# Kernel optimization log

Hardware: AMD Instinct MI355X
Metric: run time of the kernel (lower is better)

The kernel has to match this reference:

```python
import jax, jax.numpy as jnp
import numpy as np

N, E, IN, OUT, R, B = 20000, 640000, 128, 128, 65, 65
BN_EPS = 1e-5


def setup_inputs() -> dict:
    key = jax.random.key(0)
    ks = jax.random.split(key, 8)
    node_feats = jax.random.normal(ks[0], (N, IN), dtype=jnp.float32)
    src = jax.random.randint(ks[1], (E,), 0, N, dtype=jnp.int32)
    dst = jax.random.randint(ks[2], (E,), 0, N, dtype=jnp.int32)
    etype = jax.random.randint(ks[3], (E,), 0, R, dtype=jnp.int32)
    norm = jax.random.uniform(ks[4], (E, 1), dtype=jnp.float32)
    basis = jax.random.normal(ks[5], (B, IN, OUT), dtype=jnp.float32) * 0.05
    comp = jax.random.normal(ks[6], (R, B), dtype=jnp.float32) * 0.1
    h_bias = jnp.zeros((OUT,), dtype=jnp.float32)
    W_res = jax.random.normal(ks[7], (IN, OUT), dtype=jnp.float32) * 0.05
    b_res = jnp.zeros((OUT,), dtype=jnp.float32)
    gamma = jnp.ones((OUT,), dtype=jnp.float32)
    beta = jnp.zeros((OUT,), dtype=jnp.float32)
    return dict(node_feats=node_feats, src=src, dst=dst, etype=etype, norm=norm,
                basis=basis, comp=comp, h_bias=h_bias, W_res=W_res, b_res=b_res,
                gamma=gamma, beta=beta)


def reference(node_feats, src, dst, etype, norm, basis, comp, h_bias, W_res, b_res, gamma, beta):
    n, in_f = node_feats.shape
    r = comp.shape[0]
    # Basis decomposition: W_r = sum_b comp[r,b] * basis[b]  -> (R, in, out)
    W = jnp.einsum('rb,bio->rio', comp, basis)
    # Per-edge message x[src] * norm (norm is scalar per edge so it commutes
    # with the relation matmul). Aggregate per (dst, relation) first, then do
    # one dense relation-batched GEMM (mathematically identical to DGL's
    # per-edge transform + scatter-add, since everything is linear).
    msg = node_feats[src] * norm                       # (E, in)
    seg = dst.astype(jnp.int32) * r + etype            # combined (dst, rel) key
    S = jax.ops.segment_sum(msg, seg, num_segments=n * r).reshape(n, r, in_f)
    h = jnp.einsum('nri,rio->no', S, W) + h_bias       # (N, out)
    h = jax.nn.relu(h)                                 # conv activation (dropout p=0)
    # Residual branch: relu(Linear(x))
    h = h + jax.nn.relu(node_feats @ W_res + b_res)
    # BatchNorm1d (training mode: batch stats, biased variance)
    mean = jnp.mean(h, axis=0)
    var = jnp.var(h, axis=0)
    h = (h - mean) * jax.lax.rsqrt(var + BN_EPS) * gamma + beta
    return h
```

## Files before the change

kernel.cpp:

```cpp
#include <hip/hip_runtime.h>
#include <hip/hip_bf16.h>


#define N_NODES 20000
#define E_EDGES 640000
#define R_REL   65
#define TM      64
#define NB_RESID 313
#define MAX_TILES 10240
#define SCAT_CH 2560

typedef __attribute__((ext_vector_type(8))) short bf16x8;
typedef __attribute__((ext_vector_type(4))) float f32x4;
typedef __attribute__((ext_vector_type(4))) unsigned int u32x4;
typedef __attribute__((ext_vector_type(2))) unsigned int u32x2;

__device__ __forceinline__ unsigned short f2bf(float x) {
    union { float f; unsigned int u; } c; c.f = x;
    unsigned int b = c.u + 0x7fffu + ((c.u >> 16) & 1u);
    return (unsigned short)(b >> 16);
}
__device__ __forceinline__ float bf2f_lo(unsigned int u) {
    union { unsigned int u; float f; } c; c.u = u << 16; return c.f;
}
__device__ __forceinline__ float bf2f_hi(unsigned int u) {
    union { unsigned int u; float f; } c; c.u = u & 0xffff0000u; return c.f;
}
__device__ __forceinline__ void async16(const void* g, void* l) {
    __builtin_amdgcn_global_load_lds(
        (const __attribute__((address_space(1))) unsigned int*)g,
        (__attribute__((address_space(3))) unsigned int*)l, 16, 0, 0);
}
__device__ __forceinline__ int unperm(int p) {
    return (p & 64) + ((p & 3) << 4) + ((p >> 2) & 15);
}

__global__ void k_prep1(const float* __restrict__ comp, const float* __restrict__ basis,
                        float* __restrict__ W32, const int* __restrict__ et,
                        const int* __restrict__ dstA, int* __restrict__ ghist,
                        int* __restrict__ gh2, const float* __restrict__ node_feats,
                        unsigned short* __restrict__ node_bf) {
    __shared__ float lc[16 * 65];
    __shared__ int lh[R_REL];
    int b = blockIdx.x, t = threadIdx.x;
    if (b < 320) {
        int r0 = (b >> 6) * 16;
        int col = (b & 63) * 256 + t;
        for (int j = t; j < 16 * 65; j += 256) {
            int rr = r0 + j / 65;
            lc[j] = (rr < R_REL) ? comp[rr * 65 + (j % 65)] : 0.f;
        }
        __syncthreads();
        float acc[16];
#pragma unroll
        for (int j = 0; j < 16; ++j) acc[j] = 0.f;
        for (int k = 0; k < 65; ++k) {
            float v = basis[k * 16384 + col];
#pragma unroll
            for (int j = 0; j < 16; ++j) acc[j] += lc[j * 65 + k] * v;
        }
#pragma unroll
        for (int j = 0; j < 16; ++j) {
            int rr = r0 + j;
            if (rr < R_REL) W32[rr * 16384 + col] = acc[j];
        }
    } else if (b < 832) {
        if (t < R_REL) lh[t] = 0;
        __syncthreads();
        for (int i = (b - 320) * 256 + t; i < E_EDGES; i += 512 * 256) {
            atomicAdd(&lh[et[i]], 1);
            atomicAdd(&gh2[dstA[i]], 1);
        }
        __syncthreads();
        if (t < R_REL) atomicAdd(&ghist[t], lh[t]);
    } else {
        int i = (b - 832) * 256 + t;
        if (i < N_NODES * 32) {
            float4 v = reinterpret_cast<const float4*>(node_feats)[i];
            __hip_bfloat162 b0 = __float22bfloat162_rn(make_float2(v.x, v.y));
            __hip_bfloat162 b1 = __float22bfloat162_rn(make_float2(v.z, v.w));
            u32x2 pk;
            pk.x = *reinterpret_cast<unsigned int*>(&b0);
            pk.y = *reinterpret_cast<unsigned int*>(&b1);
            reinterpret_cast<u32x2*>(node_bf)[i] = pk;
        }
    }
}

__global__ void k_prep3(const int* __restrict__ gh2, int* __restrict__ cnt2,
                        int* __restrict__ seg, const int* __restrict__ ghist,
                        int* __restrict__ cnt, int* __restrict__ ntiles_p,
                        int* __restrict__ tile_rel, int* __restrict__ tile_start,
                        int* __restrict__ tile_len, const float* __restrict__ W32,
                        unsigned short* __restrict__ Wt, const float* __restrict__ Wresf,
                        unsigned short* __restrict__ Wrest) {
    int b = blockIdx.x, t = threadIdx.x;
    if (b < 80) {
        __shared__ int red[256];
        __shared__ int pref;
        int acc = 0;
        for (int i = t; i < b * 256; i += 256) acc += gh2[i];
        red[t] = acc;
        __syncthreads();
        for (int off = 128; off > 0; off >>= 1) {
            if (t < off) red[t] += red[t + off];
            __syncthreads();
        }
        if (t == 0) pref = red[0];
        __syncthreads();
        int i = b * 256 + t;
        int v = (i < N_NODES) ? gh2[i] : 0;
        red[t] = v;
        __syncthreads();
        for (int off = 1; off < 256; off <<= 1) {
            int x = (t >= off) ? red[t - off] : 0;
            __syncthreads();
            red[t] += x;
            __syncthreads();
        }
        int excl = red[t] - v + pref;
        if (i < N_NODES) {
            cnt2[i] = excl;
            seg[i] = excl;
            if (i == N_NODES - 1) seg[N_NODES] = excl + v;
        }
    } else if (b == 80) {
        __shared__ int base[R_REL + 1], tbase[R_REL + 1];
        int lane = t & 63;
        if (t < 64) {
            int v = ghist[lane];
            int x = v;
#pragma unroll
            for (int off = 1; off < 64; off <<= 1) {
                int y = __shfl_up(x, off);
                if (lane >= off) x += y;
            }
            base[lane] = x - v;
            if (lane == 63) {
                base[64] = x;
                base[65] = x + ghist[64];
            }
        }
        __syncthreads();
        if (t == 0) {
            int tb = 0;
            for (int r = 0; r < R_REL; ++r) {
                tbase[r] = tb;
                tb += (base[r + 1] - base[r] + TM - 1) / TM;
            }
            *ntiles_p = tb;
        }
        __syncthreads();
        if (t < R_REL) {
            cnt[t] = base[t];
            int s = base[t], e = base[t + 1], j = tbase[t];
            while (s < e) {
                int len = min(TM, e - s);
                tile_rel[j] = t; tile_start[j] = s; tile_len[j] = len;
                ++j; s += len;
            }
        }
    } else {
        __shared__ float tile[64][65];
        int bb = b - 81;
        const float* s; unsigned short* d; int sub;
        if (bb < R_REL * 4) { s = W32 + (size_t)(bb >> 2) * 16384; d = Wt + (size_t)(bb >> 2) * 16384; sub = bb & 3; }
        else { s = Wresf; d = Wrest; sub = bb - R_REL * 4; }
        int ot = (sub >> 1) & 1, itl = sub & 1;
        int tx = t & 63, ty = t >> 6;
        for (int it = 0; it < 16; ++it) {
            int i = ty + it * 4;
            tile[i][tx] = s[(itl * 64 + i) * 128 + ot * 64 + tx];
        }
        __syncthreads();
        for (int it = 0; it < 16; ++it) {
            int o = ty + it * 4;
            d[(ot * 64 + o) * 128 + itl * 64 + tx] = f2bf(tile[tx][o]);
        }
    }
}

__global__ void k_scatter2(const int* __restrict__ et, const int* __restrict__ srcA,
                           const int* __restrict__ dstA, const float* __restrict__ norm,
                           int* __restrict__ cnt, int* __restrict__ cnt2,
                           int* __restrict__ srcp, float* __restrict__ normp,
                           int* __restrict__ inv2) {
    __shared__ int lh[R_REL], lbase[R_REL];
    int c0 = blockIdx.x * SCAT_CH;
    int cend = min(c0 + SCAT_CH, E_EDGES);
    if (threadIdx.x < R_REL) lh[threadIdx.x] = 0;
    __syncthreads();
    for (int i = c0 + threadIdx.x; i < cend; i += 256) atomicAdd(&lh[et[i]], 1);
    __syncthreads();
    if (threadIdx.x < R_REL && lh[threadIdx.x] > 0)
        lbase[threadIdx.x] = atomicAdd(&cnt[threadIdx.x], lh[threadIdx.x]);
    __syncthreads();
    if (threadIdx.x < R_REL) lh[threadIdx.x] = 0;
    __syncthreads();
    for (int i = c0 + threadIdx.x; i < cend; i += 256) {
        int r = et[i];
        int p = lbase[r] + atomicAdd(&lh[r], 1);
        srcp[p] = srcA[i];
        normp[p] = norm[i];
        inv2[p] = atomicAdd(&cnt2[dstA[i]], 1);
    }
}

__global__ __launch_bounds__(256, 3) void k_conv_gemm(
    const int* __restrict__ tile_rel, const int* __restrict__ tile_start,
    const int* __restrict__ tile_len, const int* __restrict__ ntiles_p,
    const int* __restrict__ srcp, const float* __restrict__ normp,
    const unsigned short* __restrict__ node_bf,
    const unsigned short* __restrict__ Wt, const unsigned short* __restrict__ Wrest,
    const float* __restrict__ b_res, const int* __restrict__ inv2,
    unsigned short* __restrict__ t_out, float* __restrict__ resid) {
    __shared__ unsigned short Alds[64 * 128];
    __shared__ unsigned short Blds[128 * 128];
    __shared__ float snorm[64];
    __shared__ int sp2[64];
    int t = threadIdx.x;
    int w = t >> 6, lane = t & 63;
    int wr = (w >> 1) * 32, wc = (w & 1) * 64;
    int lrow = lane & 15, quad = lane >> 4;

    if (blockIdx.x < NB_RESID) {
        int row0 = blockIdx.x * 64;
        int nrows = min(64, N_NODES - row0);
#pragma unroll
        for (int it = 0; it < 8; ++it) {
            int j = t + 256 * it;
            int o = j >> 4, c = j & 15, cs = c ^ (o & 15);
            async16(Wrest + o * 128 + cs * 8, &Blds[o * 128 + c * 8]);
        }
#pragma unroll
        for (int it = 0; it < 4; ++it) {
            int j = t + 256 * it;
            int p = j >> 4, c = j & 15, cs = c ^ (p & 15);
            if (p < nrows)
                async16(node_bf + (size_t)(row0 + p) * 128 + cs * 8,
                        &Alds[p * 128 + c * 8]);
        }
        __syncthreads();
        f32x4 acc[2][4];
#pragma unroll
        for (int i = 0; i < 2; ++i)
#pragma unroll
            for (int j = 0; j < 4; ++j) acc[i][j] = (f32x4){0.f, 0.f, 0.f, 0.f};
#pragma unroll
        for (int ks = 0; ks < 4; ++ks) {
            int cs = (ks * 4 + quad) ^ lrow;
            bf16x8 af[2], bfr[4];
#pragma unroll
            for (int i = 0; i < 2; ++i)
                af[i] = *reinterpret_cast<const bf16x8*>(&Alds[(wr + i * 16 + lrow) * 128 + cs * 8]);
#pragma unroll
            for (int j = 0; j < 4; ++j)
                bfr[j] = *reinterpret_cast<const bf16x8*>(&Blds[(wc + j * 16 + lrow) * 128 + cs * 8]);
#pragma unroll
            for (int i = 0; i < 2; ++i)
#pragma unroll
                for (int j = 0; j < 4; ++j)
                    acc[i][j] = __builtin_amdgcn_mfma_f32_16x16x32_bf16(af[i], bfr[j], acc[i][j], 0, 0, 0);
        }
        float br0 = b_res[wc + lrow];
        float br1 = b_res[wc + 16 + lrow];
        float br2 = b_res[wc + 32 + lrow];
        float br3 = b_res[wc + 48 + lrow];
#pragma unroll
        for (int i = 0; i < 2; ++i) {
#pragma unroll
            for (int reg = 0; reg < 4; ++reg) {
                int grow = row0 + wr + i * 16 + quad * 4 + reg;
                if (grow < N_NODES) {
                    float4 v;
                    v.x = fmaxf(acc[i][0][reg] + br0, 0.f);
                    v.y = fmaxf(acc[i][1][reg] + br1, 0.f);
                    v.z = fmaxf(acc[i][2][reg] + br2, 0.f);
                    v.w = fmaxf(acc[i][3][reg] + br3, 0.f);
                    *reinterpret_cast<float4*>(resid + (size_t)grow * 128 + wc + lrow * 4) = v;
                }
            }
        }
        return;
    }

    int tid = blockIdx.x - NB_RESID;
    if (tid >= *ntiles_p) return;
    int r = tile_rel[tid], start = tile_start[tid], len = tile_len[tid];
    const unsigned short* Wr = Wt + (size_t)r * 16384;
#pragma unroll
    for (int it = 0; it < 8; ++it) {
        int j = t + 256 * it;
        int o = j >> 4, c = j & 15, cs = c ^ (o & 15);
        async16(Wr + o * 128 + cs * 8, &Blds[o * 128 + c * 8]);
    }
#pragma unroll
    for (int it = 0; it < 4; ++it) {
        int j = t + 256 * it;
        int p = j >> 4, c = j & 15, cs = c ^ (p & 15);
        if (p < len)
            async16(node_bf + (size_t)srcp[start + p] * 128 + cs * 8,
                    &Alds[p * 128 + c * 8]);
    }
    if (t < TM && t < len) {
        snorm[t] = normp[start + t];
        sp2[t] = inv2[start + t];
    }
    __syncthreads();

    f32x4 acc[2][4];
#pragma unroll
    for (int i = 0; i < 2; ++i)
#pragma unroll
        for (int j = 0; j < 4; ++j) acc[i][j] = (f32x4){0.f, 0.f, 0.f, 0.f};
#pragma unroll
    for (int ks = 0; ks < 4; ++ks) {
        int cs = (ks * 4 + quad) ^ lrow;
        bf16x8 af[2], bfr[4];
#pragma unroll
        for (int i = 0; i < 2; ++i)
            af[i] = *reinterpret_cast<const bf16x8*>(&Alds[(wr + i * 16 + lrow) * 128 + cs * 8]);
#pragma unroll
        for (int j = 0; j < 4; ++j)
            bfr[j] = *reinterpret_cast<const bf16x8*>(&Blds[(wc + j * 16 + lrow) * 128 + cs * 8]);
#pragma unroll
        for (int i = 0; i < 2; ++i)
#pragma unroll
            for (int j = 0; j < 4; ++j)
                acc[i][j] = __builtin_amdgcn_mfma_f32_16x16x32_bf16(af[i], bfr[j], acc[i][j], 0, 0, 0);
    }

#pragma unroll
    for (int i = 0; i < 2; ++i) {
        int m0 = wr + i * 16 + quad * 4;
#pragma unroll
        for (int reg = 0; reg < 4; ++reg) {
            int m = m0 + reg;
            if (m < len) {
                float nm = snorm[m];
                int p2 = sp2[m];
                float2 lo2 = make_float2(acc[i][0][reg] * nm, acc[i][1][reg] * nm);
                float2 hi2 = make_float2(acc[i][2][reg] * nm, acc[i][3][reg] * nm);
                __hip_bfloat162 blo = __float22bfloat162_rn(lo2);
                __hip_bfloat162 bhi = __float22bfloat162_rn(hi2);
                u32x2 st;
                st.x = *reinterpret_cast<unsigned int*>(&blo);
                st.y = *reinterpret_cast<unsigned int*>(&bhi);
                *reinterpret_cast<u32x2*>(t_out + (size_t)p2 * 128 + wc + lrow * 4) = st;
            }
        }
    }
}

__global__ __launch_bounds__(256) void k_reduce_fused(
    const unsigned short* __restrict__ t, const int* __restrict__ seg,
    const float* __restrict__ resid, const float* __restrict__ h_bias,
    float* __restrict__ h, float* __restrict__ colsum, float* __restrict__ colsumsq) {
    __shared__ float cs1[128], cs2[128], sbias[128];
    if (threadIdx.x < 128) {
        cs1[threadIdx.x] = 0.f; cs2[threadIdx.x] = 0.f;
        sbias[threadIdx.x] = h_bias[unperm(threadIdx.x)];
    }
    __syncthreads();
    int w = threadIdx.x >> 6, lane = threadIdx.x & 63;
    int g = lane >> 4, c = lane & 15;
    for (int k = 0; k < 4; ++k) {
        int d = blockIdx.x * 16 + k * 4 + w;
        int a = seg[d], b = seg[d + 1];
        float s[8];
#pragma unroll
        for (int kk = 0; kk < 8; ++kk) s[kk] = 0.f;
        int q = a + g;
        for (; q + 28 < b; q += 32) {
            u32x4 v0 = *reinterpret_cast<const u32x4*>(t + (size_t)q * 128 + c * 8);
            u32x4 v1 = *reinterpret_cast<const u32x4*>(t + (size_t)(q + 4) * 128 + c * 8);
            u32x4 v2 = *reinterpret_cast<const u32x4*>(t + (size_t)(q + 8) * 128 + c * 8);
            u32x4 v3 = *reinterpret_cast<const u32x4*>(t + (size_t)(q + 12) * 128 + c * 8);
            u32x4 v4 = *reinterpret_cast<const u32x4*>(t + (size_t)(q + 16) * 128 + c * 8);
            u32x4 v5 = *reinterpret_cast<const u32x4*>(t + (size_t)(q + 20) * 128 + c * 8);
            u32x4 v6 = *reinterpret_cast<const u32x4*>(t + (size_t)(q + 24) * 128 + c * 8);
            u32x4 v7 = *reinterpret_cast<const u32x4*>(t + (size_t)(q + 28) * 128 + c * 8);
#pragma unroll
            for (int kk = 0; kk < 4; ++kk) {
                s[2 * kk]     += bf2f_lo(v0[kk]) + bf2f_lo(v1[kk]) + bf2f_lo(v2[kk]) + bf2f_lo(v3[kk])
                               + bf2f_lo(v4[kk]) + bf2f_lo(v5[kk]) + bf2f_lo(v6[kk]) + bf2f_lo(v7[kk]);
                s[2 * kk + 1] += bf2f_hi(v0[kk]) + bf2f_hi(v1[kk]) + bf2f_hi(v2[kk]) + bf2f_hi(v3[kk])
                               + bf2f_hi(v4[kk]) + bf2f_hi(v5[kk]) + bf2f_hi(v6[kk]) + bf2f_hi(v7[kk]);
            }
        }
        for (; q < b; q += 4) {
            u32x4 v = *reinterpret_cast<const u32x4*>(t + (size_t)q * 128 + c * 8);
#pragma unroll
            for (int kk = 0; kk < 4; ++kk) {
                s[2 * kk]     += bf2f_lo(v[kk]);
                s[2 * kk + 1] += bf2f_hi(v[kk]);
            }
        }
#pragma unroll
        for (int kk = 0; kk < 8; ++kk) {
            s[kk] += __shfl_xor(s[kk], 16);
            s[kk] += __shfl_xor(s[kk], 32);
        }
        if (g == 0) {
            const float* rp = resid + (size_t)d * 128 + c * 8;
            float4 r0 = *reinterpret_cast<const float4*>(rp);
            float4 r1 = *reinterpret_cast<const float4*>(rp + 4);
            float rr[8] = {r0.x, r0.y, r0.z, r0.w, r1.x, r1.y, r1.z, r1.w};
            float v[8];
#pragma unroll
            for (int kk = 0; kk < 8; ++kk)
                v[kk] = fmaxf(s[kk] + sbias[c * 8 + kk], 0.f) + rr[kk];
            float* hp = h + (size_t)d * 128 + c * 8;
            *reinterpret_cast<float4*>(hp)     = make_float4(v[0], v[1], v[2], v[3]);
            *reinterpret_cast<float4*>(hp + 4) = make_float4(v[4], v[5], v[6], v[7]);
#pragma unroll
            for (int kk = 0; kk < 8; ++kk) {
                atomicAdd(&cs1[c * 8 + kk], v[kk]);
                atomicAdd(&cs2[c * 8 + kk], v[kk] * v[kk]);
            }
        }
    }
    __syncthreads();
    if (threadIdx.x < 128) {
        atomicAdd(&colsum[threadIdx.x], cs1[threadIdx.x]);
        atomicAdd(&colsumsq[threadIdx.x], cs2[threadIdx.x]);
    }
}

__global__ void k_bn(float* __restrict__ h, const float* __restrict__ colsum,
                     const float* __restrict__ colsumsq, const float* __restrict__ gamma,
                     const float* __restrict__ beta) {
    __shared__ float sc[128], sh[128], tile[8][128];
    int t = threadIdx.x;
    if (t < 128) {
        int n = unperm(t);
        float m = colsum[t] * (1.f / N_NODES);
        float var = colsumsq[t] * (1.f / N_NODES) - m * m;
        float s = gamma[n] * rsqrtf(var + 1e-5f);
        sc[t] = s;
        sh[t] = beta[n] - m * s;
    }
    __syncthreads();
    int r = t >> 5;
    int p0 = (t & 31) * 4;
    int n0 = (p0 & 64) + ((p0 >> 2) & 15);
    for (int row0 = blockIdx.x * 8; row0 < N_NODES; row0 += gridDim.x * 8) {
        int row = row0 + r;
        float4 v = make_float4(0.f, 0.f, 0.f, 0.f);
        if (row < N_NODES) v = *reinterpret_cast<float4*>(h + (size_t)row * 128 + p0);
        v.x = v.x * sc[p0] + sh[p0];
        v.y = v.y * sc[p0 + 1] + sh[p0 + 1];
        v.z = v.z * sc[p0 + 2] + sh[p0 + 2];
        v.w = v.w * sc[p0 + 3] + sh[p0 + 3];
        tile[r][n0]      = v.x;
        tile[r][n0 + 16] = v.y;
        tile[r][n0 + 32] = v.z;
        tile[r][n0 + 48] = v.w;
        __syncthreads();
        if (row < N_NODES)
            *reinterpret_cast<float4*>(h + (size_t)row * 128 + p0) =
                *reinterpret_cast<float4*>(&tile[r][p0]);
        __syncthreads();
    }
}

extern "C" void kernel_launch(void* const* d_in, const int* in_sizes, int n_in,
                              void* d_out, int out_size, void* d_ws, size_t ws_size,
                              hipStream_t stream) {
    (void)in_sizes; (void)n_in; (void)out_size; (void)ws_size;
    const float* node_feats = (const float*)d_in[0];
    const int* src    = (const int*)d_in[1];
    const int* dst    = (const int*)d_in[2];
    const int* etype  = (const int*)d_in[3];
    const float* norm = (const float*)d_in[4];
    const float* basis = (const float*)d_in[5];
    const float* comp  = (const float*)d_in[6];
    const float* h_bias = (const float*)d_in[7];
    const float* W_res  = (const float*)d_in[8];
    const float* b_res  = (const float*)d_in[9];
    const float* gamma  = (const float*)d_in[10];
    const float* beta   = (const float*)d_in[11];

    char* ws = (char*)d_ws;
    int* ghist      = (int*)(ws + 0);
    int* cnt        = (int*)(ws + 1024);
    int* ntiles_p   = (int*)(ws + 2048);
    float* colsum   = (float*)(ws + 2560);
    float* colsumsq = (float*)(ws + 3072);
    int* gh2        = (int*)(ws + 8192);
    int* tile_rel   = (int*)(ws + 88192);
    int* tile_start = (int*)(ws + 129152);
    int* tile_len   = (int*)(ws + 170112);
    unsigned short* Wt      = (unsigned short*)(ws + 211072);
    unsigned short* Wrest   = (unsigned short*)(ws + 2340992);
    unsigned short* node_bf = (unsigned short*)(ws + 2373760);
    int* srcp       = (int*)(ws + 7493760);
    float* normp    = (float*)(ws + 10053760);
    int* inv2       = (int*)(ws + 12613760);
    float* resid    = (float*)(ws + 15173760);
    int* seg        = (int*)(ws + 25413760);
    int* cnt2       = (int*)(ws + 25493776);
    const long T_BASE = 25573776L;
    float* W32      = (float*)(ws + T_BASE);
    unsigned short* t_buf = (unsigned short*)(ws + T_BASE);
    float* hacc = (float*)d_out;

    hipMemsetAsync(ws, 0, 88192, stream);
    k_prep1<<<3332, 256, 0, stream>>>(comp, basis, W32, etype, dst, ghist, gh2,
                                      node_feats, node_bf);
    k_prep3<<<345, 256, 0, stream>>>(gh2, cnt2, seg, ghist, cnt, ntiles_p,
                                     tile_rel, tile_start, tile_len,
                                     W32, Wt, W_res, Wrest);
    k_scatter2<<<(E_EDGES + SCAT_CH - 1) / SCAT_CH, 256, 0, stream>>>(
        etype, src, dst, norm, cnt, cnt2, srcp, normp, inv2);
    k_conv_gemm<<<NB_RESID + MAX_TILES, 256, 0, stream>>>(
        tile_rel, tile_start, tile_len, ntiles_p, srcp, normp, node_bf,
        Wt, Wrest, b_res, inv2, t_buf, resid);
    k_reduce_fused<<<N_NODES / 16, 256, 0, stream>>>(t_buf, seg, resid, h_bias,
                                                     hacc, colsum, colsumsq);
    k_bn<<<2500, 256, 0, stream>>>(hacc, colsum, colsumsq, gamma, beta);
}
```

Measured before the change: 323.0 us.

## Pack edge metadata and rebalance per-node reduction into edge-range sequential sweeps

The scatter now writes each edge's destination slot and norm as one packed 8-byte record, which the conv GEMM reads with a single load instead of two separate arrays. The per-node reduction is replaced by a kernel where each wavefront takes a fixed range of edge rows (found by binary search over seg) and walks it sequentially, emitting node rows as boundaries are crossed. Column statistics are kept in registers and added to shared memory only once per wavefront. Scatter chunk size is also reduced. This balances work across wavefronts regardless of node degree, at the cost of narrower 4-byte loads per lane and serial boundary handling.

```diff
diff --git a/kernel.cpp b/kernel.cpp
--- a/kernel.cpp
+++ b/kernel.cpp
@@ -8,7 +8,9 @@
 #define TM      64
 #define NB_RESID 313
 #define MAX_TILES 10240
-#define SCAT_CH 2560
+#define SCAT_CH 1024
+#define RED_BLOCKS 1000
+#define RL 160
 
 typedef __attribute__((ext_vector_type(8))) short bf16x8;
 typedef __attribute__((ext_vector_type(4))) float f32x4;
@@ -183,8 +185,7 @@
 __global__ void k_scatter2(const int* __restrict__ et, const int* __restrict__ srcA,
                            const int* __restrict__ dstA, const float* __restrict__ norm,
                            int* __restrict__ cnt, int* __restrict__ cnt2,
-                           int* __restrict__ srcp, float* __restrict__ normp,
-                           int* __restrict__ inv2) {
+                           int* __restrict__ srcp, unsigned int* __restrict__ em) {
     __shared__ int lh[R_REL], lbase[R_REL];
     int c0 = blockIdx.x * SCAT_CH;
     int cend = min(c0 + SCAT_CH, E_EDGES);
@@ -201,19 +202,21 @@
         int r = et[i];
         int p = lbase[r] + atomicAdd(&lh[r], 1);
         srcp[p] = srcA[i];
-        normp[p] = norm[i];
-        inv2[p] = atomicAdd(&cnt2[dstA[i]], 1);
+        int p2 = atomicAdd(&cnt2[dstA[i]], 1);
+        union { float f; unsigned int u; } c; c.f = norm[i];
+        u32x2 e; e.x = (unsigned int)p2; e.y = c.u;
+        *reinterpret_cast<u32x2*>(em + (size_t)p * 2) = e;
     }
 }
 
 __global__ __launch_bounds__(256, 3) void k_conv_gemm(
     const int* __restrict__ tile_rel, const int* __restrict__ tile_start,
     const int* __restrict__ tile_len, const int* __restrict__ ntiles_p,
-    const int* __restrict__ srcp, const float* __restrict__ normp,
+    const int* __restrict__ srcp, const unsigned int* __restrict__ em,
     const unsigned short* __restrict__ node_bf,
     const unsigned short* __restrict__ Wt, const unsigned short* __restrict__ Wrest,
-    const float* __restrict__ b_res, const int* __restrict__ inv2,
-    unsigned short* __restrict__ t_out, float* __restrict__ resid) {
+    const float* __restrict__ b_res, unsigned short* __restrict__ t_out,
+    float* __restrict__ resid) {
     __shared__ unsigned short Alds[64 * 128];
     __shared__ unsigned short Blds[128 * 128];
     __shared__ float snorm[64];
@@ -302,9 +305,11 @@
             async16(node_bf + (size_t)srcp[start + p] * 128 + cs * 8,
                     &Alds[p * 128 + c * 8]);
     }
-    if (t < TM && t < len) {
-        snorm[t] = normp[start + t];
-        sp2[t] = inv2[start + t];
+    if (t < TM) {
+        u32x2 e = *reinterpret_cast<const u32x2*>(em + (size_t)(start + t) * 2);
+        sp2[t] = (int)e.x;
+        union { unsigned int u; float f; } c; c.u = e.y;
+        snorm[t] = c.f;
     }
     __syncthreads();
 
@@ -352,74 +357,69 @@
     }
 }
 
-__global__ __launch_bounds__(256) void k_reduce_fused(
+__global__ __launch_bounds__(256) void k_reduce_seq(
     const unsigned short* __restrict__ t, const int* __restrict__ seg,
     const float* __restrict__ resid, const float* __restrict__ h_bias,
     float* __restrict__ h, float* __restrict__ colsum, float* __restrict__ colsumsq) {
-    __shared__ float cs1[128], cs2[128], sbias[128];
-    if (threadIdx.x < 128) {
-        cs1[threadIdx.x] = 0.f; cs2[threadIdx.x] = 0.f;
-        sbias[threadIdx.x] = h_bias[unperm(threadIdx.x)];
-    }
+    __shared__ float cs1[128], cs2[128];
+    if (threadIdx.x < 128) { cs1[threadIdx.x] = 0.f; cs2[threadIdx.x] = 0.f; }
     __syncthreads();
     int w = threadIdx.x >> 6, lane = threadIdx.x & 63;
-    int g = lane >> 4, c = lane & 15;
-    for (int k = 0; k < 4; ++k) {
-        int d = blockIdx.x * 16 + k * 4 + w;
-        int a = seg[d], b = seg[d + 1];
-        float s[8];
-#pragma unroll
-        for (int kk = 0; kk < 8; ++kk) s[kk] = 0.f;
-        int q = a + g;
-        for (; q + 28 < b; q += 32) {
-            u32x4 v0 = *reinterpret_cast<const u32x4*>(t + (size_t)q * 128 + c * 8);
-            u32x4 v1 = *reinterpret_cast<const u32x4*>(t + (size_t)(q + 4) * 128 + c * 8);
-            u32x4 v2 = *reinterpret_cast<const u32x4*>(t + (size_t)(q + 8) * 128 + c * 8);
-            u32x4 v3 = *reinterpret_cast<const u32x4*>(t + (size_t)(q + 12) * 128 + c * 8);
-            u32x4 v4 = *reinterpret_cast<const u32x4*>(t + (size_t)(q + 16) * 128 + c * 8);
-            u32x4 v5 = *reinterpret_cast<const u32x4*>(t + (size_t)(q + 20) * 128 + c * 8);
-            u32x4 v6 = *reinterpret_cast<const u32x4*>(t + (size_t)(q + 24) * 128 + c * 8);
-            u32x4 v7 = *reinterpret_cast<const u32x4*>(t + (size_t)(q + 28) * 128 + c * 8);
-#pragma unroll
-            for (int kk = 0; kk < 4; ++kk) {
-                s[2 * kk]     += bf2f_lo(v0[kk]) + bf2f_lo(v1[kk]) + bf2f_lo(v2[kk]) + bf2f_lo(v3[kk])
-                               + bf2f_lo(v4[kk]) + bf2f_lo(v5[kk]) + bf2f_lo(v6[kk]) + bf2f_lo(v7[kk]);
-                s[2 * kk + 1] += bf2f_hi(v0[kk]) + bf2f_hi(v1[kk]) + bf2f_hi(v2[kk]) + bf2f_hi(v3[kk])
-                               + bf2f_hi(v4[kk]) + bf2f_hi(v5[kk]) + bf2f_hi(v6[kk]) + bf2f_hi(v7[kk]);
-            }
-        }
-        for (; q < b; q += 4) {
-            u32x4 v = *reinterpret_cast<const u32x4*>(t + (size_t)q * 128 + c * 8);
-#pragma unroll
-            for (int kk = 0; kk < 4; ++kk) {
-                s[2 * kk]     += bf2f_lo(v[kk]);
-                s[2 * kk + 1] += bf2f_hi(v[kk]);
-            }
-        }
-#pragma unroll
-        for (int kk = 0; kk < 8; ++kk) {
-            s[kk] += __shfl_xor(s[kk], 16);
-            s[kk] += __shfl_xor(s[kk], 32);
-        }
-        if (g == 0) {
-            const float* rp = resid + (size_t)d * 128 + c * 8;
-            float4 r0 = *reinterpret_cast<const float4*>(rp);
-            float4 r1 = *reinterpret_cast<const float4*>(rp + 4);
-            float rr[8] = {r0.x, r0.y, r0.z, r0.w, r1.x, r1.y, r1.z, r1.w};
-            float v[8];
-#pragma unroll
-            for (int kk = 0; kk < 8; ++kk)
-                v[kk] = fmaxf(s[kk] + sbias[c * 8 + kk], 0.f) + rr[kk];
-            float* hp = h + (size_t)d * 128 + c * 8;
-            *reinterpret_cast<float4*>(hp)     = make_float4(v[0], v[1], v[2], v[3]);
-            *reinterpret_cast<float4*>(hp + 4) = make_float4(v[4], v[5], v[6], v[7]);
-#pragma unroll
-            for (int kk = 0; kk < 8; ++kk) {
-                atomicAdd(&cs1[c * 8 + kk], v[kk]);
-                atomicAdd(&cs2[c * 8 + kk], v[kk] * v[kk]);
-            }
-        }
-    }
+    int W = blockIdx.x * 4 + w;
+    float bias0 = h_bias[unperm(lane * 2)];
+    float bias1 = h_bias[unperm(lane * 2 + 1)];
+    float st0 = 0.f, stq0 = 0.f, st1 = 0.f, stq1 = 0.f;
+    int a = W * RL;
+    int lo = 0, hi = N_NODES;
+    while (lo < hi) { int mid = (lo + hi) >> 1; if (seg[mid] < a) lo = mid + 1; else hi = mid; }
+    int d = lo;
+    lo = d; hi = N_NODES;
+    while (lo < hi) { int mid = (lo + hi) >> 1; if (seg[mid] < a + RL) lo = mid + 1; else hi = mid; }
+    int dend = lo;
+    if (d < dend) {
+        int qstart = seg[d], qend = seg[dend];
+        int nb = seg[d + 1];
+        float s0 = 0.f, s1 = 0.f;
+        for (int base = qstart; base < qend; base += 8) {
+            unsigned int v[8];
+#pragma unroll
+            for (int i = 0; i < 8; ++i)
+                v[i] = (base + i < E_EDGES)
+                    ? reinterpret_cast<const unsigned int*>(t + (size_t)(base + i) * 128)[lane]
+                    : 0u;
+#pragma unroll
+            for (int i = 0; i < 8; ++i) {
+                int qq = base + i;
+                if (qq >= qend) break;
+                while (qq == nb) {
+                    const float* rp = resid + (size_t)d * 128 + lane * 2;
+                    float2 rr = *reinterpret_cast<const float2*>(rp);
+                    float v0 = fmaxf(s0 + bias0, 0.f) + rr.x;
+                    float v1 = fmaxf(s1 + bias1, 0.f) + rr.y;
+                    *reinterpret_cast<float2*>(h + (size_t)d * 128 + lane * 2) = make_float2(v0, v1);
+                    st0 += v0; stq0 += v0 * v0; st1 += v1; stq1 += v1 * v1;
+                    s0 = 0.f; s1 = 0.f;
+                    ++d; nb = seg[d + 1];
+                }
+                s0 += bf2f_lo(v[i]);
+                s1 += bf2f_hi(v[i]);
+            }
+        }
+        while (d < dend) {
+            const float* rp = resid + (size_t)d * 128 + lane * 2;
+            float2 rr = *reinterpret_cast<const float2*>(rp);
+            float v0 = fmaxf(s0 + bias0, 0.f) + rr.x;
+            float v1 = fmaxf(s1 + bias1, 0.f) + rr.y;
+            *reinterpret_cast<float2*>(h + (size_t)d * 128 + lane * 2) = make_float2(v0, v1);
+            st0 += v0; stq0 += v0 * v0; st1 += v1; stq1 += v1 * v1;
+            s0 = 0.f; s1 = 0.f;
+            ++d;
+        }
+    }
+    atomicAdd(&cs1[lane * 2], st0);
+    atomicAdd(&cs2[lane * 2], stq0);
+    atomicAdd(&cs1[lane * 2 + 1], st1);
+    atomicAdd(&cs2[lane * 2 + 1], stq1);
     __syncthreads();
     if (threadIdx.x < 128) {
         atomicAdd(&colsum[threadIdx.x], cs1[threadIdx.x]);
@@ -495,12 +495,11 @@
     unsigned short* Wrest   = (unsigned short*)(ws + 2340992);
     unsigned short* node_bf = (unsigned short*)(ws + 2373760);
     int* srcp       = (int*)(ws + 7493760);
-    float* normp    = (float*)(ws + 10053760);
-    int* inv2       = (int*)(ws + 12613760);
-    float* resid    = (float*)(ws + 15173760);
-    int* seg        = (int*)(ws + 25413760);
-    int* cnt2       = (int*)(ws + 25493776);
-    const long T_BASE = 25573776L;
+    unsigned int* em = (unsigned int*)(ws + 10054016);
+    float* resid    = (float*)(ws + 15174528);
+    int* seg        = (int*)(ws + 25414528);
+    int* cnt2       = (int*)(ws + 25494544);
+    const long T_BASE = 25574544L;
     float* W32      = (float*)(ws + T_BASE);
     unsigned short* t_buf = (unsigned short*)(ws + T_BASE);
     float* hacc = (float*)d_out;
@@ -512,11 +511,11 @@
                                      tile_rel, tile_start, tile_len,
                                      W32, Wt, W_res, Wrest);
     k_scatter2<<<(E_EDGES + SCAT_CH - 1) / SCAT_CH, 256, 0, stream>>>(
-        etype, src, dst, norm, cnt, cnt2, srcp, normp, inv2);
+        etype, src, dst, norm, cnt, cnt2, srcp, em);
     k_conv_gemm<<<NB_RESID + MAX_TILES, 256, 0, stream>>>(
-        tile_rel, tile_start, tile_len, ntiles_p, srcp, normp, node_bf,
-        Wt, Wrest, b_res, inv2, t_buf, resid);
-    k_reduce_fused<<<N_NODES / 16, 256, 0, stream>>>(t_buf, seg, resid, h_bias,
-                                                     hacc, colsum, colsumsq);
+        tile_rel, tile_start, tile_len, ntiles_p, srcp, em, node_bf,
+        Wt, Wrest, b_res, t_buf, resid);
+    k_reduce_seq<<<RED_BLOCKS, 256, 0, stream>>>(t_buf, seg, resid, h_bias,
+                                                 hacc, colsum, colsumsq);
     k_bn<<<2500, 256, 0, stream>>>(hacc, colsum, colsumsq, gamma, beta);
 }
```

New measurement: 336.6 us. 1.04x slower.
